# Kernel tuning notes

Measured on AMD Instinct MI355X. Metric: run time of the kernel, lower is better.

Reference implementation:

```python
import jax, jax.numpy as jnp
import numpy as np

BN_EPS = 1e-5
K = 3  # kernel size


def conv2d(x, w, b, pad):
    y = jax.lax.conv_general_dilated(
        x, w, window_strides=(1, 1), padding=[(pad, pad), (pad, pad)],
        dimension_numbers=('NCHW', 'OIHW', 'NCHW'))
    return y + b[None, :, None, None]


def setup_inputs() -> dict:
    key = jax.random.key(0)
    ks = jax.random.split(key, 4)
    B, C, H, W, O = 8, 256, 64, 64, 256
    x = jax.random.normal(ks[0], (B, C, H, W), dtype=jnp.float32)
    # offset/mask conv: 3*dg*k*k = 27 out channels; small init -> small offsets
    w_off = jax.random.normal(ks[1], (27, C, K, K), dtype=jnp.float32) * 0.01
    b_off = jnp.zeros((27,), dtype=jnp.float32)
    # main deformable conv weight/bias
    w = jax.random.normal(ks[2], (O, C, K, K), dtype=jnp.float32) * 0.05
    b = jnp.zeros((O,), dtype=jnp.float32)
    # BatchNorm (inference) params / running stats
    gamma = jnp.ones((O,), dtype=jnp.float32)
    beta = jnp.zeros((O,), dtype=jnp.float32)
    run_mean = jnp.zeros((O,), dtype=jnp.float32)
    run_var = jnp.ones((O,), dtype=jnp.float32)
    return {"x": x, "w_off": w_off, "b_off": b_off, "w": w, "b": b,
            "gamma": gamma, "beta": beta, "run_mean": run_mean, "run_var": run_var}


def _dcn_bn_relu(x, w_off, b_off, w, b, gamma, beta, run_mean, run_var):
    B, C, H, W = x.shape
    KK = K * K
    # offset + modulation mask (DCNv2): channels [0:9]=dy, [9:18]=dx, [18:27]=mask
    om = conv2d(x, w_off, b_off, pad=1)            # [B, 27, H, W]
    dy, dx = om[:, :KK], om[:, KK:2 * KK]          # [B, 9, H, W]
    mod = jax.nn.sigmoid(om[:, 2 * KK:])           # [B, 9, H, W]

    ky, kx = jnp.meshgrid(jnp.arange(K), jnp.arange(K), indexing='ij')
    # base sampling grid: out pixel + dilation*(k - center), padding=1
    base_y = jnp.arange(H, dtype=jnp.float32)[None, :, None] - 1.0 + ky.reshape(KK, 1, 1)
    base_x = jnp.arange(W, dtype=jnp.float32)[None, None, :] - 1.0 + kx.reshape(KK, 1, 1)
    py = base_y[None] + dy                          # [B, 9, H, W]
    px = base_x[None] + dx

    y0 = jnp.floor(py); x0 = jnp.floor(px)
    fy = py - y0; fx = px - x0
    y0 = y0.astype(jnp.int32); x0 = x0.astype(jnp.int32)

    x_flat = x.reshape(B, C, H * W)
    gather = jax.vmap(lambda xf, idx: xf[:, idx])   # ([C,HW],[9,H,W]) -> [C,9,H,W]

    def corner(yi, xi, wgt):
        valid = (yi >= 0) & (yi < H) & (xi >= 0) & (xi < W)
        idx = jnp.clip(yi, 0, H - 1) * W + jnp.clip(xi, 0, W - 1)
        val = gather(x_flat, idx)                   # [B, C, 9, H, W]
        return val * (wgt * valid.astype(wgt.dtype))[:, None]

    sampled = (corner(y0,     x0,     (1 - fy) * (1 - fx))
               + corner(y0,     x0 + 1, (1 - fy) * fx)
               + corner(y0 + 1, x0,     fy * (1 - fx))
               + corner(y0 + 1, x0 + 1, fy * fx))    # [B, C, 9, H, W]
    sampled = sampled * mod[:, None]                 # modulation

    O = w.shape[0]
    out = jnp.einsum('bckhw,ock->bohw', sampled, w.reshape(O, C, KK))
    out = out + b[None, :, None, None]

    # BatchNorm2d (inference) + ReLU
    inv = gamma / jnp.sqrt(run_var + BN_EPS)
    out = out * inv[None, :, None, None] + (beta - run_mean * inv)[None, :, None, None]
    return jax.nn.relu(out)


def reference(x, w_off, b_off, w, b, gamma, beta, run_mean, run_var):
    return _dcn_bn_relu(x, w_off, b_off, w, b, gamma, beta, run_mean, run_var)
```

## Files before the change

kernel.cpp:

```cpp
#include <hip/hip_runtime.h>
#include <math.h>

#define B_   8
#define C_   256
#define H_   64
#define W_   64
#define O_   256
#define KK_  9
#define CK_  2304
#define HW_  4096
#define BN_EPS 1e-5f

typedef __bf16 bf16x8 __attribute__((ext_vector_type(8)));
typedef float  f32x4  __attribute__((ext_vector_type(4)));

static __device__ __forceinline__ unsigned short f2bf(float f) {
    unsigned int u = __float_as_uint(f);
    unsigned int r = (u + 0x7fffu + ((u >> 16) & 1u)) >> 16;
    return (unsigned short)r;
}
static __device__ __forceinline__ unsigned int packbf2(float lo, float hi) {
    unsigned int ul = __float_as_uint(lo) + 0x8000u;
    unsigned int uh = __float_as_uint(hi) + 0x8000u;
    return __builtin_amdgcn_perm(uh, ul, 0x07060302u);
}
static __device__ __forceinline__ float bflo(unsigned int u) {
    return __uint_as_float(u << 16);
}
static __device__ __forceinline__ float bfhi(unsigned int u) {
    return __uint_as_float(u & 0xffff0000u);
}
static __device__ __forceinline__ uint2 wsum(const uint2 k[4], float4 wq) {
    float g0 = wq.x*bflo(k[0].x) + wq.y*bflo(k[1].x) + wq.z*bflo(k[2].x) + wq.w*bflo(k[3].x);
    float g1 = wq.x*bfhi(k[0].x) + wq.y*bfhi(k[1].x) + wq.z*bfhi(k[2].x) + wq.w*bfhi(k[3].x);
    float g2 = wq.x*bflo(k[0].y) + wq.y*bflo(k[1].y) + wq.z*bflo(k[2].y) + wq.w*bflo(k[3].y);
    float g3 = wq.x*bfhi(k[0].y) + wq.y*bfhi(k[1].y) + wq.z*bfhi(k[2].y) + wq.w*bfhi(k[3].y);
    uint2 pk;
    pk.x = packbf2(g0, g1);
    pk.y = packbf2(g2, g3);
    return pk;
}

__global__ __launch_bounds__(256) void prep_kernel(
    const float* __restrict__ x, const float* __restrict__ w,
    const float* __restrict__ w_off,
    unsigned short* __restrict__ xT, unsigned short* __restrict__ wKf,
    unsigned short* __restrict__ wof)
{
    __shared__ float tile[64][65];
    __shared__ float wbuf[4608];

    const int blk = blockIdx.x;
    const int tid = threadIdx.x, lane = tid & 63, tg = tid >> 6;

    if (blk < 512) {
        const int b = blk & 7, h = blk >> 3;
        const int hwb = h * W_;
#pragma unroll
        for (int ct = 0; ct < 4; ++ct) {
            const int c0 = ct * 64;
#pragma unroll
            for (int r = 0; r < 16; ++r) {
                int c_l = tg + r * 4;
                tile[c_l][lane] = x[((size_t)(b * C_ + c0 + c_l)) * HW_ + hwb + lane];
            }
            __syncthreads();
#pragma unroll
            for (int it = 0; it < 4; ++it) {
                const int hw_l = tg * 16 + it * 4 + (lane >> 4);
                const int c_l4 = (lane & 15) * 4;
                float v0 = tile[c_l4 + 0][hw_l];
                float v1 = tile[c_l4 + 1][hw_l];
                float v2 = tile[c_l4 + 2][hw_l];
                float v3 = tile[c_l4 + 3][hw_l];
                uint2 pk;
                pk.x = packbf2(v0, v1);
                pk.y = packbf2(v2, v3);
                *(uint2*)&xT[((size_t)(b * HW_ + hwb + hw_l)) * C_ + c0 + c_l4] = pk;
            }
            __syncthreads();
        }
    } else if (blk < 640) {
        const int t2 = blk - 512;
        const int NT = t2 >> 3, cb = t2 & 7;
#pragma unroll
        for (int i = 0; i < 18; ++i) {
            int j = i * 256 + tid;
            int o_l = j / 288, rest = j - o_l * 288;
            wbuf[o_l * 288 + rest] = w[(size_t)(NT * 16 + o_l) * CK_ + cb * 288 + rest];
        }
        __syncthreads();
#pragma unroll
        for (int i = 0; i < 18; ++i) {
            int d = i * 256 + tid;
            int tap = d >> 9, r5 = d & 511;
            int ln = r5 >> 3, e = r5 & 7;
            int n16 = ln & 15, q = ln >> 4;
            float val = wbuf[n16 * 288 + (q * 8 + e) * 9 + tap];
            wKf[((size_t)(NT * 72 + tap * 8 + cb) * 64 + ln) * 8 + e] = f2bf(val);
        }
    } else {
        const int t2 = blk - 640;
        const int NT = t2 >> 3, cb = t2 & 7;
#pragma unroll
        for (int i = 0; i < 18; ++i) {
            int j = i * 256 + tid;
            int o_l = j / 288, rest = j - o_l * 288;
            int o = NT * 16 + o_l;
            wbuf[o_l * 288 + rest] =
                (o < 27) ? w_off[(size_t)o * CK_ + cb * 288 + rest] : 0.f;
        }
        __syncthreads();
#pragma unroll
        for (int i = 0; i < 18; ++i) {
            int d = i * 256 + tid;
            int tap = d >> 9, r5 = d & 511;
            int ln = r5 >> 3, e = r5 & 7;
            int n16 = ln & 15, q = ln >> 4;
            float val = wbuf[n16 * 288 + (q * 8 + e) * 9 + tap];
            wof[((size_t)(NT * 72 + tap * 8 + cb) * 64 + ln) * 8 + e] = f2bf(val);
        }
    }
}

__global__ __launch_bounds__(512, 4) void dcn_fused_kernel(
    const unsigned short* __restrict__ xT, const unsigned short* __restrict__ wKf,
    const unsigned short* __restrict__ wof, const float* __restrict__ b_off,
    const float* __restrict__ bias, const float* __restrict__ gamma,
    const float* __restrict__ beta, const float* __restrict__ rmean,
    const float* __restrict__ rvar, float* __restrict__ out)
{
    __shared__ __align__(16) unsigned char smem[79360];
    unsigned short* rowbuf = (unsigned short*)smem;
    float4*  wgtv = (float4*)smem;
    ushort4* idxv = (ushort4*)(smem + 9216);
    typedef float OmbT[27][64];
    OmbT& omb = *(OmbT*)(smem + 13824);
    typedef unsigned short AbufT[2][8][4][64][8];
    AbufT& Abuf = *(AbufT*)(smem + 13824);

    const int blk = blockIdx.x;
    const int b = blk & 7, h = blk >> 3;
    const int tid = threadIdx.x, lane = tid & 63, wv = tid >> 6;
    const int m16 = lane & 15, q = lane >> 4;

    if (tid < 33) {
        *(uint4*)&rowbuf[tid * 8] = make_uint4(0u, 0u, 0u, 0u);
    } else if (tid >= 256 && tid < 289) {
        *(uint4*)&rowbuf[65 * 264 + (tid - 256) * 8] = make_uint4(0u, 0u, 0u, 0u);
    }

    const int mi_a = wv & 3, nj_a = wv >> 2;
    f32x4 oacc = {0.f, 0.f, 0.f, 0.f};
    const uint4* wof4 = (const uint4*)wof;

    for (int r = 0; r < 3; ++r) {
        const int hh = h - 1 + r;
        const bool vr = (hh >= 0) && (hh < H_);
        __syncthreads();
        if (vr) {
            const uint4* src = (const uint4*)&xT[((size_t)(b * HW_ + hh * W_)) * C_];
#pragma unroll
            for (int i = 0; i < 4; ++i) {
                const int idx8 = i * 512 + tid;
                uint4 v = src[idx8];
                const int px = idx8 >> 5, c8 = (idx8 & 31) * 8;
                *(uint4*)&rowbuf[(px + 1) * 264 + c8] = v;
            }
        }
        __syncthreads();
        if (vr) {
#pragma unroll
            for (int s = 0; s < 3; ++s) {
                const unsigned short* arow = &rowbuf[(mi_a * 16 + m16 + s) * 264 + q * 8];
#pragma unroll
                for (int cc = 0; cc < 8; ++cc) {
                    bf16x8 a = *(const bf16x8*)&arow[cc * 32];
                    uint4 braw = wof4[(size_t)(nj_a * 72 + (r * 3 + s) * 8 + cc) * 64 + lane];
                    oacc = __builtin_amdgcn_mfma_f32_16x16x32_bf16(
                        a, __builtin_bit_cast(bf16x8, braw), oacc, 0, 0, 0);
                }
            }
        }
    }
    __syncthreads();

    {
        const int t = nj_a * 16 + m16;
        if (t < 27) {
            const float bo = b_off[t];
            float s0 = oacc[0] + bo, s1 = oacc[1] + bo,
                  s2 = oacc[2] + bo, s3 = oacc[3] + bo;
            if (t >= 18) {
                s0 = 1.f / (1.f + expf(-s0));
                s1 = 1.f / (1.f + expf(-s1));
                s2 = 1.f / (1.f + expf(-s2));
                s3 = 1.f / (1.f + expf(-s3));
            }
            float4 rr; rr.x = s0; rr.y = s1; rr.z = s2; rr.w = s3;
            *(float4*)&omb[t][mi_a * 16 + q * 4] = rr;
        }
    }
    __syncthreads();

    for (int i = tid; i < 576; i += 512) {
        int p = i / 9, t = i - p * 9;
        float dy = omb[t][p];
        float dx = omb[t + 9][p];
        float md = omb[t + 18][p];
        float py = (float)(h - 1 + t / 3) + dy;
        float px = (float)(p - 1 + t % 3) + dx;
        float y0f = floorf(py), x0f = floorf(px);
        int   y0 = (int)y0f,    x0 = (int)x0f;
        float fy = py - y0f,    fx = px - x0f;
        int y0c = min(max(y0,     0), H_ - 1), y1c = min(max(y0 + 1, 0), H_ - 1);
        int x0c = min(max(x0,     0), W_ - 1), x1c = min(max(x0 + 1, 0), W_ - 1);
        float vy0 = (y0     >= 0 && y0     < H_) ? 1.f : 0.f;
        float vy1 = (y0 + 1 >= 0 && y0 + 1 < H_) ? 1.f : 0.f;
        float vx0 = (x0     >= 0 && x0     < W_) ? 1.f : 0.f;
        float vx1 = (x0 + 1 >= 0 && x0 + 1 < W_) ? 1.f : 0.f;
        wgtv[i] = make_float4((1.f - fy) * (1.f - fx) * vy0 * vx0 * md,
                              (1.f - fy) * fx         * vy0 * vx1 * md,
                              fy         * (1.f - fx) * vy1 * vx0 * md,
                              fy         * fx         * vy1 * vx1 * md);
        ushort4 uu;
        uu.x = (unsigned short)(y0c * W_ + x0c);
        uu.y = (unsigned short)(y0c * W_ + x1c);
        uu.z = (unsigned short)(y1c * W_ + x0c);
        uu.w = (unsigned short)(y1c * W_ + x1c);
        idxv[i] = uu;
    }
    __syncthreads();

    f32x4 acc[4][2];
#pragma unroll
    for (int mi = 0; mi < 4; ++mi)
#pragma unroll
        for (int nj = 0; nj < 2; ++nj)
#pragma unroll
            for (int r = 0; r < 4; ++r) acc[mi][nj][r] = 0.f;

    const uint4* wKf4 = (const uint4*)wKf;
    const char* xTbL = (const char*)xT + (size_t)(b * HW_) * (C_ * 2) + lane * 8;

    const int s_cc = lane >> 3;
    const int s_q2 = (lane >> 1) & 3;
    const int s_j0 = (lane & 1) * 4;
    const int s_xr = (s_q2 << 1) ^ s_cc;
    const int s_mi = wv >> 1;
    const int s_pb = (wv & 1) * 8;

    const int r_row = lane ^ ((lane >> 4) << 1);

#pragma unroll
    for (int g = 0; g < 4; ++g) {
        uint2 kr[2][4];
#pragma unroll
        for (int pp = 0; pp < 2; ++pp) {
            const ushort4 iq = idxv[(wv * 8 + g * 2 + pp) * 9];
            kr[pp][0] = *(const uint2*)(xTbL + ((int)iq.x << 9));
            kr[pp][1] = *(const uint2*)(xTbL + ((int)iq.y << 9));
            kr[pp][2] = *(const uint2*)(xTbL + ((int)iq.z << 9));
            kr[pp][3] = *(const uint2*)(xTbL + ((int)iq.w << 9));
        }
#pragma unroll
        for (int pp = 0; pp < 2; ++pp) {
            const float4 wq = wgtv[(wv * 8 + g * 2 + pp) * 9];
            uint2 pk = wsum(kr[pp], wq);
            const int row = ((s_pb + g * 2 + pp) ^ s_xr) | (s_q2 << 4);
            *(uint2*)&Abuf[0][s_cc][s_mi][row][s_j0] = pk;
        }
    }
    __syncthreads();

#pragma unroll 1
    for (int tap = 0; tap < 9; ++tap) {
        const int cbuf = tap & 1, nbuf = cbuf ^ 1;
        const bool pf = (tap < 8);

#pragma unroll
        for (int g = 0; g < 4; ++g) {
            uint4 br[4];
#pragma unroll
            for (int c2 = 0; c2 < 2; ++c2)
#pragma unroll
                for (int nj = 0; nj < 2; ++nj)
                    br[c2 * 2 + nj] =
                        wKf4[(size_t)((wv * 2 + nj) * 72 + tap * 8 + g * 2 + c2) * 64 + lane];

            uint2 kr[2][4];
            if (pf) {
#pragma unroll
                for (int pp = 0; pp < 2; ++pp) {
                    const ushort4 iq = idxv[(wv * 8 + g * 2 + pp) * 9 + tap + 1];
                    kr[pp][0] = *(const uint2*)(xTbL + ((int)iq.x << 9));
                    kr[pp][1] = *(const uint2*)(xTbL + ((int)iq.y << 9));
                    kr[pp][2] = *(const uint2*)(xTbL + ((int)iq.z << 9));
                    kr[pp][3] = *(const uint2*)(xTbL + ((int)iq.w << 9));
                }
            }

#pragma unroll
            for (int c2 = 0; c2 < 2; ++c2) {
                const int cc = g * 2 + c2;
                const int rr = r_row ^ cc;
                bf16x8 a[4];
#pragma unroll
                for (int mi = 0; mi < 4; ++mi)
                    a[mi] = *(const bf16x8*)&Abuf[cbuf][cc][mi][rr][0];
#pragma unroll
                for (int nj = 0; nj < 2; ++nj) {
                    bf16x8 bb = __builtin_bit_cast(bf16x8, br[c2 * 2 + nj]);
#pragma unroll
                    for (int mi = 0; mi < 4; ++mi)
                        acc[mi][nj] = __builtin_amdgcn_mfma_f32_16x16x32_bf16(
                            a[mi], bb, acc[mi][nj], 0, 0, 0);
                }
            }

            if (pf) {
#pragma unroll
                for (int pp = 0; pp < 2; ++pp) {
                    const float4 wq = wgtv[(wv * 8 + g * 2 + pp) * 9 + tap + 1];
                    uint2 pk = wsum(kr[pp], wq);
                    const int row = ((s_pb + g * 2 + pp) ^ s_xr) | (s_q2 << 4);
                    *(uint2*)&Abuf[nbuf][s_cc][s_mi][row][s_j0] = pk;
                }
            }
        }
        __syncthreads();
    }

#pragma unroll
    for (int nj = 0; nj < 2; ++nj) {
        const int o = wv * 32 + nj * 16 + (lane & 15);
        const float inv = gamma[o] * rsqrtf(rvar[o] + BN_EPS);
        const float sh  = beta[o] + (bias[o] - rmean[o]) * inv;
        float* ob = out + ((size_t)(b * O_ + o)) * HW_ + h * W_;
#pragma unroll
        for (int mi = 0; mi < 4; ++mi) {
            f32x4 v = acc[mi][nj];
            float4 r;
            r.x = fmaxf(v[0] * inv + sh, 0.f);
            r.y = fmaxf(v[1] * inv + sh, 0.f);
            r.z = fmaxf(v[2] * inv + sh, 0.f);
            r.w = fmaxf(v[3] * inv + sh, 0.f);
            *(float4*)&ob[mi * 16 + (lane >> 4) * 4] = r;
        }
    }
}

extern "C" void kernel_launch(void* const* d_in, const int* in_sizes, int n_in,
                              void* d_out, int out_size, void* d_ws, size_t ws_size,
                              hipStream_t stream) {
    const float* x     = (const float*)d_in[0];
    const float* w_off = (const float*)d_in[1];
    const float* b_off = (const float*)d_in[2];
    const float* w     = (const float*)d_in[3];
    const float* bias  = (const float*)d_in[4];
    const float* gamma = (const float*)d_in[5];
    const float* beta  = (const float*)d_in[6];
    const float* rmean = (const float*)d_in[7];
    const float* rvar  = (const float*)d_in[8];
    float* out = (float*)d_out;

    unsigned short* xT  = (unsigned short*)d_ws;
    unsigned short* wKf = xT + 8388608;
    unsigned short* wof = wKf + 589824;

    prep_kernel<<<656, 256, 0, stream>>>(x, w, w_off, xT, wKf, wof);
    dcn_fused_kernel<<<512, 512, 0, stream>>>(
        xT, wKf, wof, b_off, bias, gamma, beta, rmean, rvar, out);
}
```

Before: 177.6 us.

## Prefetch weight fragments one step ahead and widen transpose loads/stores

```diff
diff --git a/kernel.cpp b/kernel.cpp
--- a/kernel.cpp
+++ b/kernel.cpp
@@ -60,23 +60,31 @@
         for (int ct = 0; ct < 4; ++ct) {
             const int c0 = ct * 64;
 #pragma unroll
-            for (int r = 0; r < 16; ++r) {
-                int c_l = tg + r * 4;
-                tile[c_l][lane] = x[((size_t)(b * C_ + c0 + c_l)) * HW_ + hwb + lane];
+            for (int it = 0; it < 4; ++it) {
+                const int idx = it * 256 + tid;
+                const int c_l = idx >> 4, f4 = idx & 15;
+                float4 v = *(const float4*)
+                    &x[((size_t)(b * C_ + c0 + c_l)) * HW_ + hwb + f4 * 4];
+                tile[c_l][f4 * 4 + 0] = v.x;
+                tile[c_l][f4 * 4 + 1] = v.y;
+                tile[c_l][f4 * 4 + 2] = v.z;
+                tile[c_l][f4 * 4 + 3] = v.w;
             }
             __syncthreads();
 #pragma unroll
-            for (int it = 0; it < 4; ++it) {
-                const int hw_l = tg * 16 + it * 4 + (lane >> 4);
-                const int c_l4 = (lane & 15) * 4;
-                float v0 = tile[c_l4 + 0][hw_l];
-                float v1 = tile[c_l4 + 1][hw_l];
-                float v2 = tile[c_l4 + 2][hw_l];
-                float v3 = tile[c_l4 + 3][hw_l];
-                uint2 pk;
+            for (int it = 0; it < 2; ++it) {
+                const int hw_l = it * 32 + tg * 8 + (lane >> 3);
+                const int c8   = (lane & 7) * 8;
+                float v0 = tile[c8 + 0][hw_l], v1 = tile[c8 + 1][hw_l];
+                float v2 = tile[c8 + 2][hw_l], v3 = tile[c8 + 3][hw_l];
+                float v4 = tile[c8 + 4][hw_l], v5 = tile[c8 + 5][hw_l];
+                float v6 = tile[c8 + 6][hw_l], v7 = tile[c8 + 7][hw_l];
+                uint4 pk;
                 pk.x = packbf2(v0, v1);
                 pk.y = packbf2(v2, v3);
-                *(uint2*)&xT[((size_t)(b * HW_ + hwb + hw_l)) * C_ + c0 + c_l4] = pk;
+                pk.z = packbf2(v4, v5);
+                pk.w = packbf2(v6, v7);
+                *(uint4*)&xT[((size_t)(b * HW_ + hwb + hw_l)) * C_ + c0 + c8] = pk;
             }
             __syncthreads();
         }
@@ -230,7 +238,6 @@
         uu.w = (unsigned short)(y1c * W_ + x1c);
         idxv[i] = uu;
     }
-    __syncthreads();
 
     f32x4 acc[4][2];
 #pragma unroll
@@ -252,6 +259,15 @@
 
     const int r_row = lane ^ ((lane >> 4) << 1);
 
+    uint4 brc[4];
+#pragma unroll
+    for (int c2 = 0; c2 < 2; ++c2)
+#pragma unroll
+        for (int nj = 0; nj < 2; ++nj)
+            brc[c2 * 2 + nj] = wKf4[(size_t)((wv * 2 + nj) * 72 + c2) * 64 + lane];
+
+    __syncthreads();
+
 #pragma unroll
     for (int g = 0; g < 4; ++g) {
         uint2 kr[2][4];
@@ -280,13 +296,18 @@
 
 #pragma unroll
         for (int g = 0; g < 4; ++g) {
-            uint4 br[4];
-#pragma unroll
-            for (int c2 = 0; c2 < 2; ++c2)
-#pragma unroll
-                for (int nj = 0; nj < 2; ++nj)
-                    br[c2 * 2 + nj] =
-                        wKf4[(size_t)((wv * 2 + nj) * 72 + tap * 8 + g * 2 + c2) * 64 + lane];
+            uint4 brn[4];
+            const bool more = pf || (g < 3);
+            const int ntap = (g < 3) ? tap : tap + 1;
+            const int ncc0 = (g < 3) ? (g + 1) * 2 : 0;
+            if (more) {
+#pragma unroll
+                for (int c2 = 0; c2 < 2; ++c2)
+#pragma unroll
+                    for (int nj = 0; nj < 2; ++nj)
+                        brn[c2 * 2 + nj] =
+                            wKf4[(size_t)((wv * 2 + nj) * 72 + ntap * 8 + ncc0 + c2) * 64 + lane];
+            }
 
             uint2 kr[2][4];
             if (pf) {
@@ -310,7 +331,7 @@
                     a[mi] = *(const bf16x8*)&Abuf[cbuf][cc][mi][rr][0];
 #pragma unroll
                 for (int nj = 0; nj < 2; ++nj) {
-                    bf16x8 bb = __builtin_bit_cast(bf16x8, br[c2 * 2 + nj]);
+                    bf16x8 bb = __builtin_bit_cast(bf16x8, brc[c2 * 2 + nj]);
 #pragma unroll
                     for (int mi = 0; mi < 4; ++mi)
                         acc[mi][nj] = __builtin_amdgcn_mfma_f32_16x16x32_bf16(
@@ -326,6 +347,11 @@
                     const int row = ((s_pb + g * 2 + pp) ^ s_xr) | (s_q2 << 4);
                     *(uint2*)&Abuf[nbuf][s_cc][s_mi][row][s_j0] = pk;
                 }
+            }
+
+            if (more) {
+#pragma unroll
+                for (int k = 0; k < 4; ++k) brc[k] = brn[k];
             }
         }
         __syncthreads();
```

After: 187.3 us. +5.5%, slower.

## Split each output row into two 32-pixel halves to double block count

Applied to the files above, without the earlier changes.

```diff
diff --git a/kernel.cpp b/kernel.cpp
--- a/kernel.cpp
+++ b/kernel.cpp
@@ -123,24 +123,25 @@
     }
 }
 
-__global__ __launch_bounds__(512, 4) void dcn_fused_kernel(
+__global__ __launch_bounds__(512, 8) void dcn_fused_kernel(
     const unsigned short* __restrict__ xT, const unsigned short* __restrict__ wKf,
     const unsigned short* __restrict__ wof, const float* __restrict__ b_off,
     const float* __restrict__ bias, const float* __restrict__ gamma,
     const float* __restrict__ beta, const float* __restrict__ rmean,
     const float* __restrict__ rvar, float* __restrict__ out)
 {
-    __shared__ __align__(16) unsigned char smem[79360];
+    __shared__ __align__(16) unsigned char smem[39680];
     unsigned short* rowbuf = (unsigned short*)smem;
     float4*  wgtv = (float4*)smem;
-    ushort4* idxv = (ushort4*)(smem + 9216);
-    typedef float OmbT[27][64];
-    OmbT& omb = *(OmbT*)(smem + 13824);
-    typedef unsigned short AbufT[2][8][4][64][8];
-    AbufT& Abuf = *(AbufT*)(smem + 13824);
+    ushort4* idxv = (ushort4*)(smem + 4608);
+    typedef float OmbT[27][32];
+    OmbT& omb = *(OmbT*)(smem + 6912);
+    typedef unsigned short AbufT[2][8][2][64][8];
+    AbufT& Abuf = *(AbufT*)(smem + 6912);
 
     const int blk = blockIdx.x;
-    const int b = blk & 7, h = blk >> 3;
+    const int b = blk & 7, seg = blk >> 3;
+    const int h = seg >> 1, p0 = (seg & 1) * 32;
     const int tid = threadIdx.x, lane = tid & 63, wv = tid >> 6;
     const int m16 = lane & 15, q = lane >> 4;
 
@@ -150,7 +151,7 @@
         *(uint4*)&rowbuf[65 * 264 + (tid - 256) * 8] = make_uint4(0u, 0u, 0u, 0u);
     }
 
-    const int mi_a = wv & 3, nj_a = wv >> 2;
+    const int mi_a = wv & 1, nj_a = wv >> 1;
     f32x4 oacc = {0.f, 0.f, 0.f, 0.f};
     const uint4* wof4 = (const uint4*)wof;
 
@@ -169,10 +170,11 @@
             }
         }
         __syncthreads();
-        if (vr) {
+        if (vr && nj_a < 2) {
 #pragma unroll
             for (int s = 0; s < 3; ++s) {
-                const unsigned short* arow = &rowbuf[(mi_a * 16 + m16 + s) * 264 + q * 8];
+                const unsigned short* arow =
+                    &rowbuf[(p0 + mi_a * 16 + m16 + s) * 264 + q * 8];
 #pragma unroll
                 for (int cc = 0; cc < 8; ++cc) {
                     bf16x8 a = *(const bf16x8*)&arow[cc * 32];
@@ -185,7 +187,7 @@
     }
     __syncthreads();
 
-    {
+    if (nj_a < 2) {
         const int t = nj_a * 16 + m16;
         if (t < 27) {
             const float bo = b_off[t];
@@ -203,13 +205,14 @@
     }
     __syncthreads();
 
-    for (int i = tid; i < 576; i += 512) {
+    if (tid < 288) {
+        const int i = tid;
         int p = i / 9, t = i - p * 9;
         float dy = omb[t][p];
         float dx = omb[t + 9][p];
         float md = omb[t + 18][p];
         float py = (float)(h - 1 + t / 3) + dy;
-        float px = (float)(p - 1 + t % 3) + dx;
+        float px = (float)(p0 + p - 1 + t % 3) + dx;
         float y0f = floorf(py), x0f = floorf(px);
         int   y0 = (int)y0f,    x0 = (int)x0f;
         float fy = py - y0f,    fx = px - x0f;
@@ -232,9 +235,9 @@
     }
     __syncthreads();
 
-    f32x4 acc[4][2];
-#pragma unroll
-    for (int mi = 0; mi < 4; ++mi)
+    f32x4 acc[2][2];
+#pragma unroll
+    for (int mi = 0; mi < 2; ++mi)
 #pragma unroll
         for (int nj = 0; nj < 2; ++nj)
 #pragma unroll
@@ -247,29 +250,23 @@
     const int s_q2 = (lane >> 1) & 3;
     const int s_j0 = (lane & 1) * 4;
     const int s_xr = (s_q2 << 1) ^ s_cc;
-    const int s_mi = wv >> 1;
-    const int s_pb = (wv & 1) * 8;
+    const int s_mi = wv >> 2;
+    const int s_pb = (wv & 3) * 4;
 
     const int r_row = lane ^ ((lane >> 4) << 1);
 
 #pragma unroll
-    for (int g = 0; g < 4; ++g) {
-        uint2 kr[2][4];
-#pragma unroll
-        for (int pp = 0; pp < 2; ++pp) {
-            const ushort4 iq = idxv[(wv * 8 + g * 2 + pp) * 9];
-            kr[pp][0] = *(const uint2*)(xTbL + ((int)iq.x << 9));
-            kr[pp][1] = *(const uint2*)(xTbL + ((int)iq.y << 9));
-            kr[pp][2] = *(const uint2*)(xTbL + ((int)iq.z << 9));
-            kr[pp][3] = *(const uint2*)(xTbL + ((int)iq.w << 9));
-        }
-#pragma unroll
-        for (int pp = 0; pp < 2; ++pp) {
-            const float4 wq = wgtv[(wv * 8 + g * 2 + pp) * 9];
-            uint2 pk = wsum(kr[pp], wq);
-            const int row = ((s_pb + g * 2 + pp) ^ s_xr) | (s_q2 << 4);
-            *(uint2*)&Abuf[0][s_cc][s_mi][row][s_j0] = pk;
-        }
+    for (int pp = 0; pp < 4; ++pp) {
+        uint2 kr[4];
+        const ushort4 iq = idxv[(wv * 4 + pp) * 9];
+        kr[0] = *(const uint2*)(xTbL + ((int)iq.x << 9));
+        kr[1] = *(const uint2*)(xTbL + ((int)iq.y << 9));
+        kr[2] = *(const uint2*)(xTbL + ((int)iq.z << 9));
+        kr[3] = *(const uint2*)(xTbL + ((int)iq.w << 9));
+        const float4 wq = wgtv[(wv * 4 + pp) * 9];
+        uint2 pk = wsum(kr, wq);
+        const int row = ((s_pb + pp) ^ s_xr) | (s_q2 << 4);
+        *(uint2*)&Abuf[0][s_cc][s_mi][row][s_j0] = pk;
     }
     __syncthreads();
 
@@ -277,55 +274,43 @@
     for (int tap = 0; tap < 9; ++tap) {
         const int cbuf = tap & 1, nbuf = cbuf ^ 1;
         const bool pf = (tap < 8);
-
-#pragma unroll
-        for (int g = 0; g < 4; ++g) {
-            uint4 br[4];
-#pragma unroll
-            for (int c2 = 0; c2 < 2; ++c2)
-#pragma unroll
-                for (int nj = 0; nj < 2; ++nj)
-                    br[c2 * 2 + nj] =
-                        wKf4[(size_t)((wv * 2 + nj) * 72 + tap * 8 + g * 2 + c2) * 64 + lane];
-
-            uint2 kr[2][4];
-            if (pf) {
-#pragma unroll
-                for (int pp = 0; pp < 2; ++pp) {
-                    const ushort4 iq = idxv[(wv * 8 + g * 2 + pp) * 9 + tap + 1];
-                    kr[pp][0] = *(const uint2*)(xTbL + ((int)iq.x << 9));
-                    kr[pp][1] = *(const uint2*)(xTbL + ((int)iq.y << 9));
-                    kr[pp][2] = *(const uint2*)(xTbL + ((int)iq.z << 9));
-                    kr[pp][3] = *(const uint2*)(xTbL + ((int)iq.w << 9));
-                }
-            }
-
-#pragma unroll
-            for (int c2 = 0; c2 < 2; ++c2) {
-                const int cc = g * 2 + c2;
-                const int rr = r_row ^ cc;
-                bf16x8 a[4];
-#pragma unroll
-                for (int mi = 0; mi < 4; ++mi)
-                    a[mi] = *(const bf16x8*)&Abuf[cbuf][cc][mi][rr][0];
-#pragma unroll
-                for (int nj = 0; nj < 2; ++nj) {
-                    bf16x8 bb = __builtin_bit_cast(bf16x8, br[c2 * 2 + nj]);
-#pragma unroll
-                    for (int mi = 0; mi < 4; ++mi)
-                        acc[mi][nj] = __builtin_amdgcn_mfma_f32_16x16x32_bf16(
-                            a[mi], bb, acc[mi][nj], 0, 0, 0);
-                }
-            }
-
-            if (pf) {
-#pragma unroll
-                for (int pp = 0; pp < 2; ++pp) {
-                    const float4 wq = wgtv[(wv * 8 + g * 2 + pp) * 9 + tap + 1];
-                    uint2 pk = wsum(kr[pp], wq);
-                    const int row = ((s_pb + g * 2 + pp) ^ s_xr) | (s_q2 << 4);
-                    *(uint2*)&Abuf[nbuf][s_cc][s_mi][row][s_j0] = pk;
-                }
+        uint2 kr[4];
+
+#pragma unroll
+        for (int g = 0; g < 8; ++g) {
+            uint4 br[2];
+#pragma unroll
+            for (int nj = 0; nj < 2; ++nj)
+                br[nj] = wKf4[(size_t)((wv * 2 + nj) * 72 + tap * 8 + g) * 64 + lane];
+
+            if (pf && (g & 1) == 0) {
+                const ushort4 iq = idxv[(wv * 4 + (g >> 1)) * 9 + tap + 1];
+                kr[0] = *(const uint2*)(xTbL + ((int)iq.x << 9));
+                kr[1] = *(const uint2*)(xTbL + ((int)iq.y << 9));
+                kr[2] = *(const uint2*)(xTbL + ((int)iq.z << 9));
+                kr[3] = *(const uint2*)(xTbL + ((int)iq.w << 9));
+            }
+
+            const int rr = r_row ^ g;
+            bf16x8 a[2];
+#pragma unroll
+            for (int mi = 0; mi < 2; ++mi)
+                a[mi] = *(const bf16x8*)&Abuf[cbuf][g][mi][rr][0];
+#pragma unroll
+            for (int nj = 0; nj < 2; ++nj) {
+                bf16x8 bb = __builtin_bit_cast(bf16x8, br[nj]);
+#pragma unroll
+                for (int mi = 0; mi < 2; ++mi)
+                    acc[mi][nj] = __builtin_amdgcn_mfma_f32_16x16x32_bf16(
+                        a[mi], bb, acc[mi][nj], 0, 0, 0);
+            }
+
+            if (pf && (g & 1) == 1) {
+                const int pp = g >> 1;
+                const float4 wq = wgtv[(wv * 4 + pp) * 9 + tap + 1];
+                uint2 pk = wsum(kr, wq);
+                const int row = ((s_pb + pp) ^ s_xr) | (s_q2 << 4);
+                *(uint2*)&Abuf[nbuf][s_cc][s_mi][row][s_j0] = pk;
             }
         }
         __syncthreads();
@@ -333,19 +318,19 @@
 
 #pragma unroll
     for (int nj = 0; nj < 2; ++nj) {
-        const int o = wv * 32 + nj * 16 + (lane & 15);
+        const int o = wv * 32 + nj * 16 + m16;
         const float inv = gamma[o] * rsqrtf(rvar[o] + BN_EPS);
         const float sh  = beta[o] + (bias[o] - rmean[o]) * inv;
-        float* ob = out + ((size_t)(b * O_ + o)) * HW_ + h * W_;
-#pragma unroll
-        for (int mi = 0; mi < 4; ++mi) {
+        float* ob = out + ((size_t)(b * O_ + o)) * HW_ + h * W_ + p0;
+#pragma unroll
+        for (int mi = 0; mi < 2; ++mi) {
             f32x4 v = acc[mi][nj];
             float4 r;
             r.x = fmaxf(v[0] * inv + sh, 0.f);
             r.y = fmaxf(v[1] * inv + sh, 0.f);
             r.z = fmaxf(v[2] * inv + sh, 0.f);
             r.w = fmaxf(v[3] * inv + sh, 0.f);
-            *(float4*)&ob[mi * 16 + (lane >> 4) * 4] = r;
+            *(float4*)&ob[mi * 16 + q * 4] = r;
         }
     }
 }
@@ -369,6 +354,6 @@
     unsigned short* wof = wKf + 589824;
 
     prep_kernel<<<656, 256, 0, stream>>>(x, w, w_off, xT, wKf, wof);
-    dcn_fused_kernel<<<512, 512, 0, stream>>>(
+    dcn_fused_kernel<<<1024, 512, 0, stream>>>(
         xT, wKf, wof, b_off, bias, gamma, beta, rmean, rvar, out);
 }
```

Result: slower. 199.8 us (+12.5%).
